# Optimization experiments

Hardware: AMD Instinct MI355X
Metric: run time of the kernel (lower is better)

The kernel has to match this reference:

```python
import jax, jax.numpy as jnp
import numpy as np

R, K = 16, 64  # rel_size (heads), key_size (head dim)
LN_EPS = 1e-5


def apply_rope(x, pos):
    # pos: [B,S,1,K], halves are sin/cos; x: [B,S,R,K]
    sin, cos = jnp.split(pos, 2, axis=-1)
    x0, x1 = jnp.split(x, 2, axis=-1)
    return jnp.concatenate([x0 * cos - x1 * sin, x0 * sin + x1 * cos], axis=-1)


def setup_inputs() -> dict:
    key = jax.random.key(0)
    ks = jax.random.split(key, 6)
    B, S, H = 2, 2048, 1024
    x = jax.random.normal(ks[0], (B, S, H), dtype=jnp.float32)
    pos = jax.random.uniform(ks[1], (B, S, 1, K), dtype=jnp.float32)
    W_qkv = jax.random.normal(ks[2], (H, R * K * 3), dtype=jnp.float32) * (H ** -0.5)
    b_qkv = jax.random.normal(ks[3], (R * K * 3,), dtype=jnp.float32) * 0.02
    W_out = jax.random.normal(ks[4], (R * K, H), dtype=jnp.float32) * ((R * K) ** -0.5)
    b_out = jax.random.normal(ks[5], (H,), dtype=jnp.float32) * 0.02
    ln_g = jnp.ones((H,), dtype=jnp.float32)
    ln_b = jnp.zeros((H,), dtype=jnp.float32)
    return {"x": x, "pos": pos, "W_qkv": W_qkv, "b_qkv": b_qkv,
            "W_out": W_out, "b_out": b_out, "ln_g": ln_g, "ln_b": ln_b}


def reference(x, pos, W_qkv, b_qkv, W_out, b_out, ln_g, ln_b):
    B, S, H = x.shape
    qkv = (x @ W_qkv + b_qkv).reshape(B, S, R, 3 * K)
    q, k, v = jnp.split(qkv, 3, axis=-1)  # each [B,S,R,K]
    k = k / jnp.linalg.norm(k, axis=-1, keepdims=True)
    q = apply_rope(q, pos)
    k = apply_rope(k, pos)
    # SDPA with scale=1 (as in the original call)
    scores = jnp.einsum('bqhd,bkhd->bhqk', q, k)
    attn = jax.nn.softmax(scores, axis=-1)
    ctx = jnp.einsum('bhqk,bkhd->bqhd', attn, v).reshape(B, S, R * K)
    postx = ctx @ W_out + b_out
    y = x + postx
    mu = jnp.mean(y, axis=-1, keepdims=True)
    var = jnp.mean(jnp.square(y - mu), axis=-1, keepdims=True)
    return (y - mu) * jax.lax.rsqrt(var + LN_EPS) * ln_g + ln_b
```

## Files before the change

kernel.cpp:

```cpp
#include <hip/hip_runtime.h>


#define B_   2
#define S_   2048
#define H_   1024
#define R_   16
#define BS_  (B_*S_)
#define NQKV 3072
#define LOG2E 1.44269504088896f

typedef float    floatx4 __attribute__((ext_vector_type(4)));
typedef _Float16 half8   __attribute__((ext_vector_type(8)));
typedef _Float16 half4   __attribute__((ext_vector_type(4)));
typedef __fp16   fp16x2  __attribute__((ext_vector_type(2)));

#if __has_builtin(__builtin_amdgcn_exp2f)
#define EXP2(x) __builtin_amdgcn_exp2f(x)
#else
#define EXP2(x) exp2f(x)
#endif

__device__ __forceinline__ void gl_lds16(const _Float16* g, _Float16* l) {
    __builtin_amdgcn_global_load_lds(
        (const __attribute__((address_space(1))) unsigned int*)g,
        (__attribute__((address_space(3))) unsigned int*)l, 16, 0, 0);
}

__global__ __launch_bounds__(256) void prep0_kernel(
    const float* __restrict__ x, _Float16* __restrict__ x_h,
    const float* __restrict__ W_qkv, _Float16* __restrict__ wqkv_t,
    const float* __restrict__ W_out, _Float16* __restrict__ wout_t)
{
    __shared__ float tile[32][33];
    int bid = blockIdx.x, tid = threadIdx.x;
    if (bid < 4096) {
        int i = bid * 1024 + tid * 4;
        float4 v = *(const float4*)(x + i);
        half4 h;
        h.x = (_Float16)v.x; h.y = (_Float16)v.y;
        h.z = (_Float16)v.z; h.w = (_Float16)v.w;
        *(half4*)(x_h + i) = h;
        return;
    }
    const float* in; _Float16* out; int rows, cols, bx, by;
    if (bid < 7168) {
        int t = bid - 4096;
        in = W_qkv; out = wqkv_t; rows = H_; cols = NQKV;
        bx = t % 96; by = t / 96;
    } else {
        int t = bid - 7168;
        in = W_out; out = wout_t; rows = H_; cols = H_;
        bx = t & 31; by = t >> 5;
    }
    int cx = bx * 32, ry = by * 32;
    int tx = tid & 31, ty = tid >> 5;
#pragma unroll
    for (int i = 0; i < 32; i += 8)
        tile[ty + i][tx] = in[(size_t)(ry + ty + i) * cols + cx + tx];
    __syncthreads();
#pragma unroll
    for (int i = 0; i < 32; i += 8)
        out[(size_t)(cx + ty + i) * rows + ry + tx] = (_Float16)tile[tx][ty + i];
}

__global__ __launch_bounds__(256) void gemm_f16_mfma(
    const _Float16* __restrict__ A, const _Float16* __restrict__ Bt,
    const float* __restrict__ bias, _Float16* __restrict__ Ch,
    int M, int N, int Kd)
{
    __shared__ _Float16 Als[2][4096];
    __shared__ _Float16 Bls[2][4096];
    int tid  = threadIdx.x;
    int lane = tid & 63, w = tid >> 6;
    int wr = w >> 1, wc = w & 1;
    int fr = lane & 15, fq = lane >> 4;

    int nbx = gridDim.x;
    int orig = blockIdx.x + nbx * blockIdx.y;
    int nwg  = nbx * gridDim.y;
    int swz  = (nwg & 7) ? orig : ((orig & 7) * (nwg >> 3) + (orig >> 3));
    int bx = swz % nbx, by = swz / nbx;
    int m0 = by * 128, n0 = bx * 128;

    floatx4 acc[4][4] = {};

    const _Float16* ga[2]; const _Float16* gb[2];
    int loff[2];
#pragma unroll
    for (int i2 = 0; i2 < 2; ++i2) {
        int ch = 2 * w + i2;
        int row = ch * 16 + (lane >> 2), col = (lane & 3) * 8;
        ga[i2] = A  + (size_t)(m0 + row) * Kd + col;
        gb[i2] = Bt + (size_t)(n0 + row) * Kd + col;
        loff[i2] = ch * 512;
    }

    int nIter = Kd >> 5;
#pragma unroll
    for (int i2 = 0; i2 < 2; ++i2) {
        gl_lds16(ga[i2], &Als[0][loff[i2]]);
        gl_lds16(gb[i2], &Bls[0][loff[i2]]);
    }

    for (int it = 0; it < nIter; ++it) {
        int cur = it & 1;
        __syncthreads();
        if (it + 1 < nIter) {
            int k1 = (it + 1) << 5;
#pragma unroll
            for (int i2 = 0; i2 < 2; ++i2) {
                gl_lds16(ga[i2] + k1, &Als[cur ^ 1][loff[i2]]);
                gl_lds16(gb[i2] + k1, &Bls[cur ^ 1][loff[i2]]);
            }
        }
        const _Float16* Ab = Als[cur];
        const _Float16* Bb = Bls[cur];
        half8 af[4], bf[4];
#pragma unroll
        for (int i = 0; i < 4; ++i)
            af[i] = *(const half8*)(Ab + (wr * 64 + i * 16 + fr) * 32 + fq * 8);
#pragma unroll
        for (int j = 0; j < 4; ++j)
            bf[j] = *(const half8*)(Bb + (wc * 64 + j * 16 + fr) * 32 + fq * 8);
#pragma unroll
        for (int i = 0; i < 4; ++i)
#pragma unroll
            for (int j = 0; j < 4; ++j)
                acc[i][j] = __builtin_amdgcn_mfma_f32_16x16x32_f16(
                    af[i], bf[j], acc[i][j], 0, 0, 0);
    }

#pragma unroll
    for (int i = 0; i < 4; ++i)
#pragma unroll
        for (int j = 0; j < 4; ++j)
#pragma unroll
            for (int r2 = 0; r2 < 4; ++r2) {
                int row = m0 + wr * 64 + i * 16 + fq * 4 + r2;
                int col = n0 + wc * 64 + j * 16 + fr;
                Ch[(size_t)row * N + col] = (_Float16)(acc[i][j][r2] + bias[col]);
            }
}

__global__ __launch_bounds__(256) void gemm64_f16_mfma(
    const _Float16* __restrict__ A, const _Float16* __restrict__ Bt,
    const float* __restrict__ bias, const float* __restrict__ resid,
    float* __restrict__ Cf, int M, int N, int Kd)
{
    __shared__ _Float16 Als[2][2048];
    __shared__ _Float16 Bls[2][2048];
    int tid = threadIdx.x, lane = tid & 63, w = tid >> 6;
    int wr = w >> 1, wc = w & 1;
    int fr = lane & 15, fq = lane >> 4;

    int nbx = gridDim.x;
    int orig = blockIdx.x + nbx * blockIdx.y;
    int nwg  = nbx * gridDim.y;
    int swz  = (nwg & 7) ? orig : ((orig & 7) * (nwg >> 3) + (orig >> 3));
    int bx = swz % nbx, by = swz / nbx;
    int m0 = by * 64, n0 = bx * 64;

    floatx4 acc[2][2] = {};

    int srow = w * 16 + (lane >> 2), scol = (lane & 3) * 8;
    const _Float16* ga = A  + (size_t)(m0 + srow) * Kd + scol;
    const _Float16* gb = Bt + (size_t)(n0 + srow) * Kd + scol;
    int loff = w * 512;

    int nIter = Kd >> 5;
    gl_lds16(ga, &Als[0][loff]);
    gl_lds16(gb, &Bls[0][loff]);

    for (int it = 0; it < nIter; ++it) {
        int cur = it & 1;
        __syncthreads();
        if (it + 1 < nIter) {
            int k1 = (it + 1) << 5;
            gl_lds16(ga + k1, &Als[cur ^ 1][loff]);
            gl_lds16(gb + k1, &Bls[cur ^ 1][loff]);
        }
        const _Float16* Ab = Als[cur];
        const _Float16* Bb = Bls[cur];
        half8 af[2], bf[2];
#pragma unroll
        for (int i = 0; i < 2; ++i)
            af[i] = *(const half8*)(Ab + (wr * 32 + i * 16 + fr) * 32 + fq * 8);
#pragma unroll
        for (int j = 0; j < 2; ++j)
            bf[j] = *(const half8*)(Bb + (wc * 32 + j * 16 + fr) * 32 + fq * 8);
#pragma unroll
        for (int i = 0; i < 2; ++i)
#pragma unroll
            for (int j = 0; j < 2; ++j)
                acc[i][j] = __builtin_amdgcn_mfma_f32_16x16x32_f16(
                    af[i], bf[j], acc[i][j], 0, 0, 0);
    }

#pragma unroll
    for (int i = 0; i < 2; ++i)
#pragma unroll
        for (int j = 0; j < 2; ++j)
#pragma unroll
            for (int r2 = 0; r2 < 4; ++r2) {
                int row = m0 + wr * 32 + i * 16 + fq * 4 + r2;
                int col = n0 + wc * 32 + j * 16 + fr;
                Cf[(size_t)row * N + col] =
                    acc[i][j][r2] + bias[col] + resid[(size_t)row * N + col];
            }
}

__global__ __launch_bounds__(256) void prep1_kernel(
    const _Float16* __restrict__ qkvh, const float* __restrict__ pos,
    _Float16* __restrict__ qt, _Float16* __restrict__ kt,
    _Float16* __restrict__ vt2)
{
    __shared__ float tile[64][65];
    int head = blockIdx.x, tau = blockIdx.y;
    int s0 = tau * 64;
    int b = head >> 4, rh = head & 15;
    int lane = threadIdx.x & 63, w = threadIdx.x >> 6;

#pragma unroll
    for (int si = w; si < 64; si += 4)
        tile[si][lane] =
            (float)qkvh[(size_t)(b * S_ + s0 + si) * NQKV + rh * 192 + 128 + lane];
    __syncthreads();
    {
        int P = lane;
        int op = P >> 3;
        int hi = (P >> 2) & 1, lo = P & 3;
#pragma unroll
        for (int d = w; d < 64; d += 4) {
            int ol = op ^ (d & 7);
            int key = 32 * (ol >> 2) + 16 * hi + 4 * (ol & 3) + lo;
            vt2[(((size_t)head * 32 + tau) * 64 + d) * 64 + P] = (_Float16)tile[key][d];
        }
    }

    for (int i = 0; i < 16; ++i) {
        int s = s0 + w * 16 + i;
        int bs = b * S_ + s;
        const _Float16* base = qkvh + (size_t)bs * NQKV + rh * 192;
        float qv = (float)base[lane];
        float kv = (float)base[64 + lane];

        float ss = kv * kv;
#pragma unroll
        for (int off = 32; off > 0; off >>= 1) ss += __shfl_xor(ss, off);
        kv *= rsqrtf(ss);

        int j = lane & 31;
        float sn = pos[(size_t)bs * 64 + j];
        float cs = pos[(size_t)bs * 64 + 32 + j];
        float qp = __shfl_xor(qv, 32);
        float kp = __shfl_xor(kv, 32);
        float qo, ko;
        if (lane < 32) { qo = qv * cs - qp * sn; ko = kv * cs - kp * sn; }
        else           { qo = qp * sn + qv * cs; ko = kp * sn + kv * cs; }

        size_t oidx = ((size_t)head * S_ + s) * 64 + lane;
        qt[oidx] = (_Float16)(qo * LOG2E);
        kt[oidx] = (_Float16)ko;
    }
}

__global__ __launch_bounds__(256) void attn_mfma_kernel(
    const _Float16* __restrict__ qt, const _Float16* __restrict__ kt,
    const _Float16* __restrict__ vt2,
    _Float16* __restrict__ opart, float* __restrict__ lpart)
{
    __shared__ _Float16 Kls[2][8192];
    __shared__ _Float16 Vls[2][8192];

    int orig = blockIdx.x + 16 * blockIdx.y + 512 * blockIdx.z;
    int swz  = (orig & 7) * 128 + (orig >> 3);
    int q0   = (swz & 15) * 128;
    int head = (swz >> 4) & 31;
    int ks   = swz >> 9;

    int b = head >> 4, rh = head & 15;
    int tid = threadIdx.x, lane = tid & 63, w = tid >> 6;
    int g = lane >> 4, c = lane & 15;

    half8 qf[2][2];
    floatx4 mz[2];
    float mL[2], l_s[2] = {0.f, 0.f};
#pragma unroll
    for (int qg = 0; qg < 2; ++qg) {
        const _Float16* qp =
            qt + ((size_t)head * S_ + q0 + w * 32 + qg * 16 + c) * 64 + 8 * g;
        qf[qg][0] = *(const half8*)qp;
        qf[qg][1] = *(const half8*)(qp + 32);
        float qq = 0.f;
#pragma unroll
        for (int i = 0; i < 8; ++i) {
            float a = (float)qf[qg][0][i], b2 = (float)qf[qg][1][i];
            qq += a * a + b2 * b2;
        }
        qq += __shfl_xor(qq, 16);
        qq += __shfl_xor(qq, 32);
        mL[qg] = sqrtf(qq);
        float nm = -mL[qg];
        mz[qg][0] = nm; mz[qg][1] = nm; mz[qg][2] = nm; mz[qg][3] = nm;
    }

    floatx4 o_acc[2][4] = {};

    const _Float16* kg[2]; const _Float16* vg[2];
    int loff[2];
#pragma unroll
    for (int i2 = 0; i2 < 2; ++i2) {
        int ch = 2 * w + i2;
        int krow = ch * 8 + (lane >> 3);
        int koct = (lane & 7) ^ (lane >> 3);
        kg[i2] = kt + ((size_t)head * S_ + krow) * 64 + koct * 8;
        vg[i2] = vt2 + ((size_t)head * 32) * 4096 + ch * 512 + lane * 8;
        loff[i2] = ch * 512;
    }

    int co = c & 7;
    int jbase = ks << 4;

#pragma unroll
    for (int s = 0; s < 2; ++s)
#pragma unroll
        for (int i2 = 0; i2 < 2; ++i2) {
            gl_lds16(kg[i2] + (size_t)(jbase + s) * 4096,
                     &Kls[0][s * 4096 + loff[i2]]);
            gl_lds16(vg[i2] + (size_t)(jbase + s) * 4096,
                     &Vls[0][s * 4096 + loff[i2]]);
        }

    for (int jt = 0; jt < 8; ++jt) {
        int cur = jt & 1;
        __syncthreads();
        if (jt + 1 < 8) {
#pragma unroll
            for (int s = 0; s < 2; ++s) {
                size_t joff = (size_t)(jbase + 2 * (jt + 1) + s) * 4096;
#pragma unroll
                for (int i2 = 0; i2 < 2; ++i2) {
                    gl_lds16(kg[i2] + joff, &Kls[cur ^ 1][s * 4096 + loff[i2]]);
                    gl_lds16(vg[i2] + joff, &Vls[cur ^ 1][s * 4096 + loff[i2]]);
                }
            }
        }

#pragma unroll
        for (int s = 0; s < 2; ++s) {
            const _Float16* Kbuf = &Kls[cur][s * 4096];
            const _Float16* Vbuf = &Vls[cur][s * 4096];

            half8 kfr[8];
#pragma unroll
            for (int t = 0; t < 4; ++t) {
                const _Float16* krow = Kbuf + (16 * t + c) * 64;
                kfr[2 * t]     = *(const half8*)(krow + ((g) ^ co) * 8);
                kfr[2 * t + 1] = *(const half8*)(krow + ((4 + g) ^ co) * 8);
            }

            union { half8 v; fp16x2 h2[4]; } pf[2][2];
#pragma unroll
            for (int qg = 0; qg < 2; ++qg) {
                floatx4 sacc[4];
#pragma unroll
                for (int t = 0; t < 4; ++t) {
                    floatx4 z = mz[qg];
                    z = __builtin_amdgcn_mfma_f32_16x16x32_f16(
                        kfr[2 * t], qf[qg][0], z, 0, 0, 0);
                    z = __builtin_amdgcn_mfma_f32_16x16x32_f16(
                        kfr[2 * t + 1], qf[qg][1], z, 0, 0, 0);
                    sacc[t] = z;
                }
                float ps = 0.f;
#pragma unroll
                for (int t = 0; t < 4; ++t)
#pragma unroll
                    for (int r = 0; r < 4; ++r) {
                        float p = EXP2(sacc[t][r]);
                        sacc[t][r] = p;
                        ps += p;
                    }
                l_s[qg] += ps;
                pf[qg][0].h2[0] = __builtin_amdgcn_cvt_pkrtz(sacc[0][0], sacc[0][1]);
                pf[qg][0].h2[1] = __builtin_amdgcn_cvt_pkrtz(sacc[0][2], sacc[0][3]);
                pf[qg][0].h2[2] = __builtin_amdgcn_cvt_pkrtz(sacc[1][0], sacc[1][1]);
                pf[qg][0].h2[3] = __builtin_amdgcn_cvt_pkrtz(sacc[1][2], sacc[1][3]);
                pf[qg][1].h2[0] = __builtin_amdgcn_cvt_pkrtz(sacc[2][0], sacc[2][1]);
                pf[qg][1].h2[1] = __builtin_amdgcn_cvt_pkrtz(sacc[2][2], sacc[2][3]);
                pf[qg][1].h2[2] = __builtin_amdgcn_cvt_pkrtz(sacc[3][0], sacc[3][1]);
                pf[qg][1].h2[3] = __builtin_amdgcn_cvt_pkrtz(sacc[3][2], sacc[3][3]);
            }

#pragma unroll
            for (int t = 0; t < 4; ++t) {
                const _Float16* vrow = Vbuf + (16 * t + c) * 64;
                half8 v0 = *(const half8*)(vrow + ((g) ^ co) * 8);
                half8 v1 = *(const half8*)(vrow + ((4 + g) ^ co) * 8);
#pragma unroll
                for (int qg = 0; qg < 2; ++qg) {
                    o_acc[qg][t] = __builtin_amdgcn_mfma_f32_16x16x32_f16(
                        v0, pf[qg][0].v, o_acc[qg][t], 0, 0, 0);
                    o_acc[qg][t] = __builtin_amdgcn_mfma_f32_16x16x32_f16(
                        v1, pf[qg][1].v, o_acc[qg][t], 0, 0, 0);
                }
            }
        }
    }

#pragma unroll
    for (int qg = 0; qg < 2; ++qg) {
        float lt = l_s[qg];
        lt += __shfl_xor(lt, 16);
        lt += __shfl_xor(lt, 32);
        int q = q0 + w * 32 + qg * 16 + c;
        if (lane < 16)
            lpart[((size_t)ks * 32 + head) * S_ + q] = lt;
        size_t rowbase =
            ((size_t)ks * BS_ + (size_t)(b * S_ + q)) * 1024 + rh * 64;
#pragma unroll
        for (int t = 0; t < 4; ++t) {
            union { half4 v; fp16x2 h2[2]; } e;
            e.h2[0] = __builtin_amdgcn_cvt_pkrtz(o_acc[qg][t][0], o_acc[qg][t][1]);
            e.h2[1] = __builtin_amdgcn_cvt_pkrtz(o_acc[qg][t][2], o_acc[qg][t][3]);
            *(half4*)(opart + rowbase + 16 * t + 4 * g) = e.v;
        }
    }
}

__global__ __launch_bounds__(256) void merge_kernel(
    const _Float16* __restrict__ opart, const float* __restrict__ lpart,
    _Float16* __restrict__ ctx)
{
    int idx = blockIdx.x * 256 + threadIdx.x;
    int row = idx >> 7;
    int col = (idx & 127) * 8;
    int b = row >> 11, s = row & 2047;
    int head = b * 16 + (col >> 6);
    float l0 = lpart[(size_t)head * S_ + s];
    float l1 = lpart[(size_t)(32 + head) * S_ + s];
    float inv = 1.f / (l0 + l1);
    size_t off = (size_t)row * 1024 + col;
    half8 a = *(const half8*)(opart + off);
    half8 b8 = *(const half8*)(opart + (size_t)BS_ * 1024 + off);
    union { half8 v; fp16x2 h2[4]; } e;
#pragma unroll
    for (int i = 0; i < 4; ++i)
        e.h2[i] = __builtin_amdgcn_cvt_pkrtz(
            ((float)a[2 * i]     + (float)b8[2 * i])     * inv,
            ((float)a[2 * i + 1] + (float)b8[2 * i + 1]) * inv);
    *(half8*)(ctx + off) = e.v;
}

__global__ __launch_bounds__(256) void ln_kernel(
    float* __restrict__ y, const float* __restrict__ g, const float* __restrict__ bb)
{
    int row = blockIdx.x, tid = threadIdx.x;
    float* p = y + (size_t)row * 1024;
    float4 v = ((const float4*)p)[tid];
    float sum = v.x + v.y + v.z + v.w;
    float sq  = v.x*v.x + v.y*v.y + v.z*v.z + v.w*v.w;
#pragma unroll
    for (int off = 32; off > 0; off >>= 1) {
        sum += __shfl_xor(sum, off);
        sq  += __shfl_xor(sq,  off);
    }
    __shared__ float rs[4], rq[4];
    int w = tid >> 6;
    if ((tid & 63) == 0) { rs[w] = sum; rq[w] = sq; }
    __syncthreads();
    sum = rs[0] + rs[1] + rs[2] + rs[3];
    sq  = rq[0] + rq[1] + rq[2] + rq[3];
    float mean = sum * (1.f / 1024.f);
    float var  = sq * (1.f / 1024.f) - mean * mean;
    float inv  = rsqrtf(var + 1e-5f);
    float4 gv = ((const float4*)g)[tid];
    float4 bv = ((const float4*)bb)[tid];
    v.x = (v.x - mean) * inv * gv.x + bv.x;
    v.y = (v.y - mean) * inv * gv.y + bv.y;
    v.z = (v.z - mean) * inv * gv.z + bv.z;
    v.w = (v.w - mean) * inv * gv.w + bv.w;
    ((float4*)p)[tid] = v;
}

extern "C" void kernel_launch(void* const* d_in, const int* in_sizes, int n_in,
                              void* d_out, int out_size, void* d_ws, size_t ws_size,
                              hipStream_t stream)
{
    const float* x     = (const float*)d_in[0];
    const float* pos   = (const float*)d_in[1];
    const float* W_qkv = (const float*)d_in[2];
    const float* b_qkv = (const float*)d_in[3];
    const float* W_out = (const float*)d_in[4];
    const float* b_out = (const float*)d_in[5];
    const float* ln_g  = (const float*)d_in[6];
    const float* ln_b  = (const float*)d_in[7];
    float* out = (float*)d_out;

    char* ws = (char*)d_ws;
    _Float16* x_h    = (_Float16*)(ws);
    _Float16* ctx_h  = (_Float16*)(ws);
    _Float16* wqkv_t = (_Float16*)(ws + ((size_t)8  << 20));
    _Float16* wout_t = (_Float16*)(ws + ((size_t)14 << 20));
    _Float16* qkvh   = (_Float16*)(ws + ((size_t)16 << 20));
    _Float16* opart  = (_Float16*)(ws + ((size_t)16 << 20));
    float*    lpart  = (float*)   (ws + ((size_t)32 << 20));
    _Float16* qt_h   = (_Float16*)(ws + ((size_t)40 << 20));
    _Float16* kt_h   = (_Float16*)(ws + ((size_t)48 << 20));
    _Float16* vt2_h  = (_Float16*)(ws + ((size_t)56 << 20));

    prep0_kernel<<<8192, 256, 0, stream>>>(x, x_h, W_qkv, wqkv_t, W_out, wout_t);

    gemm_f16_mfma<<<dim3(NQKV / 128, BS_ / 128), 256, 0, stream>>>(
        x_h, wqkv_t, b_qkv, qkvh, BS_, NQKV, H_);

    prep1_kernel<<<dim3(32, 32), 256, 0, stream>>>(qkvh, pos, qt_h, kt_h, vt2_h);

    attn_mfma_kernel<<<dim3(16, 32, 2), 256, 0, stream>>>(
        qt_h, kt_h, vt2_h, opart, lpart);

    merge_kernel<<<2048, 256, 0, stream>>>(opart, lpart, ctx_h);

    gemm64_f16_mfma<<<dim3(H_ / 64, BS_ / 64), 256, 0, stream>>>(
        ctx_h, wout_t, b_out, x, out, BS_, H_, H_);

    ln_kernel<<<BS_, 256, 0, stream>>>(out, ln_g, ln_b);
}
```

Baseline: 221.2 us.

## Drop split-key attention and fuse normalization into attention epilogue, removing merge kernel

The attention kernel no longer splits the key range into two halves across a grid z-dimension. Each block now walks all key tiles itself and normalizes by the row sum in its epilogue, writing fp16 context directly. This removes the partial-output and partial-sum buffers and the separate merge kernel, along with their global memory round trip and one launch. In exchange the grid has half as many blocks, each with a loop twice as long, which lowers available parallelism and latency hiding.

```diff
diff --git a/kernel.cpp b/kernel.cpp
--- a/kernel.cpp
+++ b/kernel.cpp
@@ -266,17 +266,15 @@
 
 __global__ __launch_bounds__(256) void attn_mfma_kernel(
     const _Float16* __restrict__ qt, const _Float16* __restrict__ kt,
-    const _Float16* __restrict__ vt2,
-    _Float16* __restrict__ opart, float* __restrict__ lpart)
+    const _Float16* __restrict__ vt2, _Float16* __restrict__ ctx)
 {
     __shared__ _Float16 Kls[2][8192];
     __shared__ _Float16 Vls[2][8192];
 
-    int orig = blockIdx.x + 16 * blockIdx.y + 512 * blockIdx.z;
-    int swz  = (orig & 7) * 128 + (orig >> 3);
+    int orig = blockIdx.x + 16 * blockIdx.y;
+    int swz  = (orig & 7) * 64 + (orig >> 3);
     int q0   = (swz & 15) * 128;
-    int head = (swz >> 4) & 31;
-    int ks   = swz >> 9;
+    int head = swz >> 4;
 
     int b = head >> 4, rh = head & 15;
     int tid = threadIdx.x, lane = tid & 63, w = tid >> 6;
@@ -319,25 +317,22 @@
     }
 
     int co = c & 7;
-    int jbase = ks << 4;
 
 #pragma unroll
     for (int s = 0; s < 2; ++s)
 #pragma unroll
         for (int i2 = 0; i2 < 2; ++i2) {
-            gl_lds16(kg[i2] + (size_t)(jbase + s) * 4096,
-                     &Kls[0][s * 4096 + loff[i2]]);
-            gl_lds16(vg[i2] + (size_t)(jbase + s) * 4096,
-                     &Vls[0][s * 4096 + loff[i2]]);
-        }
-
-    for (int jt = 0; jt < 8; ++jt) {
+            gl_lds16(kg[i2] + (size_t)s * 4096, &Kls[0][s * 4096 + loff[i2]]);
+            gl_lds16(vg[i2] + (size_t)s * 4096, &Vls[0][s * 4096 + loff[i2]]);
+        }
+
+    for (int jt = 0; jt < 16; ++jt) {
         int cur = jt & 1;
         __syncthreads();
-        if (jt + 1 < 8) {
+        if (jt + 1 < 16) {
 #pragma unroll
             for (int s = 0; s < 2; ++s) {
-                size_t joff = (size_t)(jbase + 2 * (jt + 1) + s) * 4096;
+                size_t joff = (size_t)(2 * (jt + 1) + s) * 4096;
 #pragma unroll
                 for (int i2 = 0; i2 < 2; ++i2) {
                     gl_lds16(kg[i2] + joff, &Kls[cur ^ 1][s * 4096 + loff[i2]]);
@@ -413,43 +408,19 @@
         float lt = l_s[qg];
         lt += __shfl_xor(lt, 16);
         lt += __shfl_xor(lt, 32);
+        float inv = 1.f / lt;
         int q = q0 + w * 32 + qg * 16 + c;
-        if (lane < 16)
-            lpart[((size_t)ks * 32 + head) * S_ + q] = lt;
-        size_t rowbase =
-            ((size_t)ks * BS_ + (size_t)(b * S_ + q)) * 1024 + rh * 64;
+        size_t rowbase = (size_t)(b * S_ + q) * 1024 + rh * 64;
 #pragma unroll
         for (int t = 0; t < 4; ++t) {
             union { half4 v; fp16x2 h2[2]; } e;
-            e.h2[0] = __builtin_amdgcn_cvt_pkrtz(o_acc[qg][t][0], o_acc[qg][t][1]);
-            e.h2[1] = __builtin_amdgcn_cvt_pkrtz(o_acc[qg][t][2], o_acc[qg][t][3]);
-            *(half4*)(opart + rowbase + 16 * t + 4 * g) = e.v;
-        }
-    }
-}
-
-__global__ __launch_bounds__(256) void merge_kernel(
-    const _Float16* __restrict__ opart, const float* __restrict__ lpart,
-    _Float16* __restrict__ ctx)
-{
-    int idx = blockIdx.x * 256 + threadIdx.x;
-    int row = idx >> 7;
-    int col = (idx & 127) * 8;
-    int b = row >> 11, s = row & 2047;
-    int head = b * 16 + (col >> 6);
-    float l0 = lpart[(size_t)head * S_ + s];
-    float l1 = lpart[(size_t)(32 + head) * S_ + s];
-    float inv = 1.f / (l0 + l1);
-    size_t off = (size_t)row * 1024 + col;
-    half8 a = *(const half8*)(opart + off);
-    half8 b8 = *(const half8*)(opart + (size_t)BS_ * 1024 + off);
-    union { half8 v; fp16x2 h2[4]; } e;
-#pragma unroll
-    for (int i = 0; i < 4; ++i)
-        e.h2[i] = __builtin_amdgcn_cvt_pkrtz(
-            ((float)a[2 * i]     + (float)b8[2 * i])     * inv,
-            ((float)a[2 * i + 1] + (float)b8[2 * i + 1]) * inv);
-    *(half8*)(ctx + off) = e.v;
+            e.h2[0] = __builtin_amdgcn_cvt_pkrtz(o_acc[qg][t][0] * inv,
+                                                 o_acc[qg][t][1] * inv);
+            e.h2[1] = __builtin_amdgcn_cvt_pkrtz(o_acc[qg][t][2] * inv,
+                                                 o_acc[qg][t][3] * inv);
+            *(half4*)(ctx + rowbase + 16 * t + 4 * g) = e.v;
+        }
+    }
 }
 
 __global__ __launch_bounds__(256) void ln_kernel(
@@ -503,8 +474,6 @@
     _Float16* wqkv_t = (_Float16*)(ws + ((size_t)8  << 20));
     _Float16* wout_t = (_Float16*)(ws + ((size_t)14 << 20));
     _Float16* qkvh   = (_Float16*)(ws + ((size_t)16 << 20));
-    _Float16* opart  = (_Float16*)(ws + ((size_t)16 << 20));
-    float*    lpart  = (float*)   (ws + ((size_t)32 << 20));
     _Float16* qt_h   = (_Float16*)(ws + ((size_t)40 << 20));
     _Float16* kt_h   = (_Float16*)(ws + ((size_t)48 << 20));
     _Float16* vt2_h  = (_Float16*)(ws + ((size_t)56 << 20));
@@ -516,10 +485,8 @@
 
     prep1_kernel<<<dim3(32, 32), 256, 0, stream>>>(qkvh, pos, qt_h, kt_h, vt2_h);
 
-    attn_mfma_kernel<<<dim3(16, 32, 2), 256, 0, stream>>>(
-        qt_h, kt_h, vt2_h, opart, lpart);
-
-    merge_kernel<<<2048, 256, 0, stream>>>(opart, lpart, ctx_h);
+    attn_mfma_kernel<<<dim3(16, 32), 256, 0, stream>>>(
+        qt_h, kt_h, vt2_h, ctx_h);
 
     gemm64_f16_mfma<<<dim3(H_ / 64, BS_ / 64), 256, 0, stream>>>(
         ctx_h, wout_t, b_out, x, out, BS_, H_, H_);
```

After: 212.9 us. 1.04x faster.
